# Performance work log

Hardware: AMD Instinct MI355X
Metric: run time of the kernel (lower is better)

## Reference

```python
import jax, jax.numpy as jnp
import numpy as np
import math

NB = 4           # num_bands
EPS = 1e-5       # LayerNorm eps


def _dwconv(x, w):
    # depthwise Conv1d, padding=1, kernel=3. x: [b, t, c], w: [c, 1, k]
    c = x.shape[-1]
    y = jax.lax.conv_general_dilated(
        x.transpose(0, 2, 1), w, window_strides=(1,), padding=[(1, 1)],
        dimension_numbers=('NCH', 'OIH', 'NCH'), feature_group_count=c)
    return y.transpose(0, 2, 1)


def _ln(x, g, b):
    m = jnp.mean(x, axis=-1, keepdims=True)
    v = jnp.mean(jnp.square(x - m), axis=-1, keepdims=True)
    return (x - m) * jax.lax.rsqrt(v + EPS) * g + b


def _attn(x, mem, qw, qc, kw, kc, vw, vc, ow, pw, prev_qk):
    # x, mem: [b, w, c]
    b, w, c = x.shape
    d = c // NB
    q = _dwconv(x @ qw.T, qc).reshape(b, w, NB, d).transpose(0, 2, 1, 3)      # [b,nb,w,d]
    k = _dwconv(mem @ kw.T, kc).reshape(b, w, NB, d).transpose(0, 2, 3, 1)    # [b,nb,d,w]
    v = _dwconv(mem @ vw.T, vc).reshape(b, w, NB, d).transpose(0, 2, 1, 3)    # [b,nb,w,d]
    # skewed relative-position bias: matmul + pad + transpose + slice
    p = jnp.einsum('bnwd,dt->bnwt', q, pw[:, :w])                              # [b,nb,w,w]
    p = jnp.pad(p, ((0, 0), (0, 0), (0, 0), (1, 0)))                           # pad last dim left
    p = p.transpose(0, 1, 3, 2)[:, :, 1:, :]                                   # skew
    qk = (jnp.einsum('bnwd,bndt->bnwt', q, k) + p) / math.sqrt(c)
    if prev_qk is not None:
        qk = qk + prev_qk
    a = jnp.einsum('bnwt,bntd->bnwd', jax.nn.softmax(qk, axis=-1), v)
    a = a.transpose(0, 2, 1, 3).reshape(b, w, c)
    return a @ ow.T, qk


def setup_inputs() -> dict:
    key = jax.random.key(0)
    ks = jax.random.split(key, 32)
    B, CH, BINS, W, FF = 4, 8, 1024, 1024, 2048
    s = 0.02
    inp = {
        'x': jax.random.normal(ks[0], (B, CH, BINS, W), jnp.float32),
        'mem': jax.random.normal(ks[1], (B, CH, BINS, W), jnp.float32),
        'prev_qk1': jax.random.normal(ks[2], (B, NB, W, W), jnp.float32),
        'prev_qk2': jax.random.normal(ks[3], (B, NB, W, W), jnp.float32),
        'ip_w': jax.random.normal(ks[4], (CH,), jnp.float32) * s,
        'ip_b': jnp.zeros((1,), jnp.float32),
        'mp_w': jax.random.normal(ks[5], (CH,), jnp.float32) * s,
        'mp_b': jnp.zeros((1,), jnp.float32),
        'ln1_g': jnp.ones((BINS,), jnp.float32), 'ln1_b': jnp.zeros((BINS,), jnp.float32),
        'ln2_g': jnp.ones((BINS,), jnp.float32), 'ln2_b': jnp.zeros((BINS,), jnp.float32),
        'ln3_g': jnp.ones((BINS,), jnp.float32), 'ln3_b': jnp.zeros((BINS,), jnp.float32),
        'a1_qw': jax.random.normal(ks[6], (BINS, BINS), jnp.float32) * s,
        'a1_qc': jax.random.normal(ks[7], (BINS, 1, 3), jnp.float32) * 0.3,
        'a1_kw': jax.random.normal(ks[8], (BINS, BINS), jnp.float32) * s,
        'a1_kc': jax.random.normal(ks[9], (BINS, 1, 3), jnp.float32) * 0.3,
        'a1_vw': jax.random.normal(ks[10], (BINS, BINS), jnp.float32) * s,
        'a1_vc': jax.random.normal(ks[11], (BINS, 1, 3), jnp.float32) * 0.3,
        'a1_ow': jax.random.normal(ks[12], (BINS, BINS), jnp.float32) * s,
        'a1_pw': jax.random.normal(ks[13], (BINS // NB, W), jnp.float32),
        'a2_qw': jax.random.normal(ks[14], (BINS, BINS), jnp.float32) * s,
        'a2_qc': jax.random.normal(ks[15], (BINS, 1, 3), jnp.float32) * 0.3,
        'a2_kw': jax.random.normal(ks[16], (BINS, BINS), jnp.float32) * s,
        'a2_kc': jax.random.normal(ks[17], (BINS, 1, 3), jnp.float32) * 0.3,
        'a2_vw': jax.random.normal(ks[18], (BINS, BINS), jnp.float32) * s,
        'a2_vc': jax.random.normal(ks[19], (BINS, 1, 3), jnp.float32) * 0.3,
        'a2_ow': jax.random.normal(ks[20], (BINS, BINS), jnp.float32) * s,
        'a2_pw': jax.random.normal(ks[21], (BINS // NB, W), jnp.float32),
        'l1_w': jax.random.normal(ks[22], (FF, BINS), jnp.float32) * s,
        'l2_w': jax.random.normal(ks[23], (BINS, FF), jnp.float32) * s,
    }
    return inp


def reference(x, mem, prev_qk1, prev_qk2, ip_w, ip_b, mp_w, mp_b,
              ln1_g, ln1_b, ln2_g, ln2_b, ln3_g, ln3_b,
              a1_qw, a1_qc, a1_kw, a1_kc, a1_vw, a1_vc, a1_ow, a1_pw,
              a2_qw, a2_qc, a2_kw, a2_kc, a2_vw, a2_vc, a2_ow, a2_pw,
              l1_w, l2_w):
    # 1x1 Conv2d to 1 channel then [b, w, bins] layout
    xs = jnp.einsum('bchw,c->bwh', x, ip_w) + ip_b    # [b, w, bins]
    ms = jnp.einsum('bchw,c->bwh', mem, mp_w) + mp_b
    # self-attention with prev_qk residual
    h, qk1 = _attn(_ln(xs, ln1_g, ln1_b), _ln(xs, ln1_g, ln1_b),
                   a1_qw, a1_qc, a1_kw, a1_kc, a1_vw, a1_vc, a1_ow, a1_pw, prev_qk1)
    xs = xs + h
    # cross-attention against mem
    h, qk2 = _attn(_ln(xs, ln2_g, ln2_b), ms,
                   a2_qw, a2_qc, a2_kw, a2_kc, a2_vw, a2_vc, a2_ow, a2_pw, prev_qk2)
    xs = xs + h
    # squared-ReLU FFN
    h = _ln(xs, ln3_g, ln3_b)
    h = jnp.square(jax.nn.relu(h @ l1_w.T)) @ l2_w.T
    xs = xs + h
    out = xs.transpose(0, 2, 1)[:, None]              # [b, 1, bins, w]
    return (out, qk1, qk2)
```

## Files before the change

### kernel.cpp

```cpp
#include <hip/hip_runtime.h>
#include <stdint.h>

typedef unsigned short u16;
typedef __bf16 bfv8 __attribute__((ext_vector_type(8)));
typedef float f32x4 __attribute__((ext_vector_type(4)));
typedef unsigned short u16x8 __attribute__((ext_vector_type(8)));

#define DI __device__ __forceinline__

DI u16 f2bf(float f) {
  union { float f; unsigned u; } c; c.f = f;
  unsigned r = c.u + 0x7FFFu + ((c.u >> 16) & 1u);
  return (u16)(r >> 16);
}
DI float bf2f(u16 b) {
  union { unsigned u; float f; } c; c.u = ((unsigned)b) << 16;
  return c.f;
}

enum { EPI_BF16 = 0, EPI_RELU2 = 1, EPI_ADDF32 = 2, EPI_QK = 3 };

#define GLDS(g, l)                                                              \
  __builtin_amdgcn_global_load_lds((const __attribute__((address_space(1))) void*)(g), \
                                   (__attribute__((address_space(3))) void*)(l), 16, 0, 0)

#define VMCNT_BAR(N)                                        \
  do {                                                      \
    asm volatile("s_waitcnt vmcnt(" #N ")" ::: "memory");   \
    __builtin_amdgcn_sched_barrier(0);                      \
    __builtin_amdgcn_s_barrier();                           \
    __builtin_amdgcn_sched_barrier(0);                      \
  } while (0)

template <int EPI, bool KSPLIT, int BN>
__global__ __launch_bounds__(512) void gemm256(
    const u16* __restrict__ Aq, const u16* __restrict__ Akv, int asplit,
    long a1q, long a1r, int lda1,
    const u16* __restrict__ A2, int lda2,
    const u16* __restrict__ B1, long b1q, long b1r, int ldb1,
    const u16* __restrict__ B2, long b2q, long b2r, int ldb2,
    int K, int ksp,
    void* __restrict__ Cv, long cq, long cr, int ldc,
    const float* __restrict__ extra, long eq, int lde,
    float scale)
{
  constexpr int NJ = BN / 64;
  constexpr int NBL = BN / 64;
  constexpr int SS = 8192 + BN * 64;
  constexpr int LPS = 2 + NBL;
  __shared__ __align__(16) u16 lds[3 * SS];
  const int tid = threadIdx.x;
  const int wid = tid >> 6, lane = tid & 63;

  const int gx = gridDim.x, gy = gridDim.y;
  const int nwg = gx * gy * (int)gridDim.z;
  const int flat = blockIdx.x + gx * (blockIdx.y + gy * blockIdx.z);
  const int q = nwg >> 3, r = nwg & 7;
  const int xcd = flat & 7, idx = flat >> 3;
  const int wg = (xcd < r ? xcd * (q + 1) : r * (q + 1) + (xcd - r) * q) + idx;
  const int bx = wg % gx;
  const int tmp = wg / gx;
  const int by = tmp % gy;
  const int bz = tmp / gy;

  const long zq = bz >> 2, zr = bz & 3;
  const int m0 = by * 128, n0 = bx * BN;
  const u16* Ab = ((n0 >= asplit) ? Akv : Aq) + zq * a1q + zr * a1r;
  const u16* Bb = B1 + zq * b1q + zr * b1r;
  const u16* B2b = KSPLIT ? (B2 + zq * b2q + zr * b2r) : (const u16*)nullptr;
  const int wm = (wid >> 2) * 64, wn = (wid & 3) * (BN / 4);
  const int fr = lane & 15, fq = lane >> 4;

  f32x4 acc[4][NJ];
#pragma unroll
  for (int i = 0; i < 4; ++i)
#pragma unroll
    for (int j = 0; j < NJ; ++j)
      acc[i][j] = (f32x4){0.f, 0.f, 0.f, 0.f};

  const int nt = K >> 6;

  auto STAGE = [&](int tt, int sb) {
    const int k0 = tt << 6;
    u16* Ld = &lds[sb * SS];
    const u16* Asrc; int la; const u16* Bsrc; int lb;
    if (!KSPLIT || k0 < ksp) { Asrc = Ab + k0; la = lda1; Bsrc = Bb + k0; lb = ldb1; }
    else { Asrc = A2 + (k0 - ksp); la = lda2; Bsrc = B2b + (k0 - ksp); lb = ldb2; }
#pragma unroll
    for (int l = 0; l < 2; ++l) {
      int idx2 = (l << 9) + tid;
      int row = idx2 >> 3;
      int sc = ((idx2 & 7) ^ (row & 7)) << 3;
      GLDS(Asrc + (size_t)(m0 + row) * la + sc,
           Ld + (((l << 3) + wid) << 9));
    }
#pragma unroll
    for (int l = 0; l < NBL; ++l) {
      int idx2 = (l << 9) + tid;
      int row = idx2 >> 3;
      int sc = ((idx2 & 7) ^ (row & 7)) << 3;
      GLDS(Bsrc + (size_t)(n0 + row) * lb + sc,
           Ld + 8192 + (((l << 3) + wid) << 9));
    }
  };

  auto COMPUTE = [&](int cb) {
    const u16* As = &lds[cb * SS];
    const u16* Bs = As + 8192;
#pragma unroll
    for (int ks = 0; ks < 2; ++ks) {
      bfv8 av[4];
#pragma unroll
      for (int i = 0; i < 4; ++i) {
        int ra = wm + i * 16 + fr;
        int ca = (((ks << 2) + fq) ^ (ra & 7)) << 3;
        av[i] = *(const bfv8*)&As[(ra << 6) + ca];
      }
#pragma unroll
      for (int nh = 0; nh < NJ / 2; ++nh) {
        bfv8 bv[2];
#pragma unroll
        for (int j = 0; j < 2; ++j) {
          int rb = wn + (nh << 5) + (j << 4) + fr;
          int cb2 = (((ks << 2) + fq) ^ (rb & 7)) << 3;
          bv[j] = *(const bfv8*)&Bs[(rb << 6) + cb2];
        }
        __builtin_amdgcn_s_setprio(1);
#pragma unroll
        for (int i = 0; i < 4; ++i) {
          acc[i][(nh << 1)] = __builtin_amdgcn_mfma_f32_16x16x32_bf16(av[i], bv[0], acc[i][(nh << 1)], 0, 0, 0);
          acc[i][(nh << 1) + 1] = __builtin_amdgcn_mfma_f32_16x16x32_bf16(av[i], bv[1], acc[i][(nh << 1) + 1], 0, 0, 0);
        }
        __builtin_amdgcn_s_setprio(0);
      }
    }
  };

  STAGE(0, 0);
  STAGE(1, 1);
  if constexpr (LPS == 6) VMCNT_BAR(6); else VMCNT_BAR(4);
  int cur = 0;
  for (int t = 0; t < nt; ++t) {
    if (t + 2 < nt) {
      int stg = cur + 2; if (stg >= 3) stg -= 3;
      STAGE(t + 2, stg);
      COMPUTE(cur);
      if constexpr (LPS == 6) VMCNT_BAR(6); else VMCNT_BAR(4);
    } else if (t + 1 < nt) {
      COMPUTE(cur);
      VMCNT_BAR(0);
    } else {
      COMPUTE(cur);
    }
    cur = (cur == 2) ? 0 : cur + 1;
  }

  if constexpr (EPI == EPI_BF16 || EPI == EPI_RELU2) {
    u16* Cb = (u16*)Cv + zq * cq + zr * cr;
#pragma unroll
    for (int i = 0; i < 4; ++i)
#pragma unroll
      for (int j = 0; j < NJ; ++j)
#pragma unroll
        for (int r2 = 0; r2 < 4; ++r2) {
          int row = m0 + wm + i * 16 + (fq << 2) + r2;
          int col = n0 + wn + j * 16 + fr;
          float v = acc[i][j][r2];
          if constexpr (EPI == EPI_RELU2) { v = fmaxf(v, 0.f); v = v * v; }
          Cb[(size_t)row * ldc + col] = f2bf(v);
        }
  } else if constexpr (EPI == EPI_ADDF32) {
    float* Cb = (float*)Cv + zq * cq + zr * cr;
#pragma unroll
    for (int i = 0; i < 4; ++i)
#pragma unroll
      for (int j = 0; j < NJ; ++j)
#pragma unroll
        for (int r2 = 0; r2 < 4; ++r2) {
          int row = m0 + wm + i * 16 + (fq << 2) + r2;
          int col = n0 + wn + j * 16 + fr;
          Cb[(size_t)row * ldc + col] += acc[i][j][r2];
        }
  } else {
    float* Cb = (float*)Cv + zq * cq + zr * cr;
    const float* Eb = extra + (size_t)bz * eq;
#pragma unroll
    for (int i = 0; i < 4; ++i)
#pragma unroll
      for (int j = 0; j < NJ; ++j)
#pragma unroll
        for (int r2 = 0; r2 < 4; ++r2) {
          int row = m0 + wm + i * 16 + (fq << 2) + r2;
          int col = n0 + wn + j * 16 + fr;
          Cb[(size_t)row * ldc + col] = acc[i][j][r2] * scale + Eb[(size_t)row * lde + col];
        }
  }
}

__global__ __launch_bounds__(1024) void proj3_kernel(const float* __restrict__ x,
                                                     const float* __restrict__ memp,
                                                     const float* __restrict__ ipw,
                                                     const float* __restrict__ ipb,
                                                     const float* __restrict__ mpw,
                                                     const float* __restrict__ mpb,
                                                     float* __restrict__ xs,
                                                     u16* __restrict__ msb)
{
  __shared__ f32x4 lt[16][256];
  const int task = blockIdx.z;
  const int b = blockIdx.y;
  const int h0 = blockIdx.x * 16;
  const float* src = task ? memp : x;
  const float* w8 = task ? mpw : ipw;
  const float bias = task ? mpb[0] : ipb[0];
  const int t = threadIdx.x;
  const int w4 = t & 255, hl = t >> 8;
  float wr[8];
#pragma unroll
  for (int c = 0; c < 8; ++c) wr[c] = w8[c];
#pragma unroll
  for (int p = 0; p < 4; ++p) {
    const int hr = p * 4 + hl;
    const size_t rowbase = ((size_t)b * 8 * 1024 + (h0 + hr)) * 1024 + (w4 << 2);
    f32x4 acc = {bias, bias, bias, bias};
#pragma unroll
    for (int c = 0; c < 8; ++c) {
      f32x4 v = *(const f32x4*)&src[rowbase + (size_t)c * 1048576];
      acc.x += v.x * wr[c]; acc.y += v.y * wr[c]; acc.z += v.z * wr[c]; acc.w += v.w * wr[c];
    }
    lt[hr][w4] = acc;
  }
  __syncthreads();
  const int w = t;
  float o[16];
#pragma unroll
  for (int h = 0; h < 16; ++h)
    o[h] = ((const float*)&lt[h][0])[w];
  if (task) {
    u16* d = &msb[((size_t)b * 1024 + w) * 1024 + h0];
    u16x8 o0, o1;
#pragma unroll
    for (int h = 0; h < 8; ++h) { o0[h] = f2bf(o[h]); o1[h] = f2bf(o[h + 8]); }
    *(u16x8*)&d[0] = o0;
    *(u16x8*)&d[8] = o1;
  } else {
    float* d = &xs[((size_t)b * 1024 + w) * 1024 + h0];
#pragma unroll
    for (int p = 0; p < 4; ++p) {
      f32x4 v = {o[p * 4], o[p * 4 + 1], o[p * 4 + 2], o[p * 4 + 3]};
      *(f32x4*)&d[p * 4] = v;
    }
  }
}

__global__ __launch_bounds__(256) void ln_kernel(const float* __restrict__ x,
                                                 const float* __restrict__ g,
                                                 const float* __restrict__ b,
                                                 u16* __restrict__ out)
{
  int row = blockIdx.x, tid = threadIdx.x;
  float4 v = ((const float4*)(x + (size_t)row * 1024))[tid];
  float s = v.x + v.y + v.z + v.w;
  float s2 = v.x * v.x + v.y * v.y + v.z * v.z + v.w * v.w;
#pragma unroll
  for (int o = 32; o; o >>= 1) { s += __shfl_down(s, o); s2 += __shfl_down(s2, o); }
  __shared__ float rs[4], rs2[4];
  int wid = tid >> 6, lane = tid & 63;
  if (lane == 0) { rs[wid] = s; rs2[wid] = s2; }
  __syncthreads();
  s = rs[0] + rs[1] + rs[2] + rs[3];
  s2 = rs2[0] + rs2[1] + rs2[2] + rs2[3];
  float mean = s * (1.f / 1024.f);
  float var = s2 * (1.f / 1024.f) - mean * mean;
  float rstd = rsqrtf(var + 1e-5f);
  float4 gv = ((const float4*)g)[tid];
  float4 bv = ((const float4*)b)[tid];
  ushort4 o;
  o.x = f2bf((v.x - mean) * rstd * gv.x + bv.x);
  o.y = f2bf((v.y - mean) * rstd * gv.y + bv.y);
  o.z = f2bf((v.z - mean) * rstd * gv.z + bv.z);
  o.w = f2bf((v.w - mean) * rstd * gv.w + bv.w);
  ((ushort4*)out)[(size_t)row * 256 + tid] = o;
}

__global__ __launch_bounds__(128) void dwconv_qk_kernel(const u16* __restrict__ qkv,
                                                        const float* __restrict__ qc,
                                                        const float* __restrict__ kc,
                                                        u16* __restrict__ Qc,
                                                        u16* __restrict__ Kc)
{
  int sel = blockIdx.y;
  int row = blockIdx.x;
  int t = row & 1023;
  int c0 = threadIdx.x * 8;
  const u16* r0 = qkv + (size_t)row * 3072 + (sel << 10) + c0;
  const float* wc = sel ? kc : qc;
  u16* dst = (sel ? Kc : Qc) + (size_t)row * 1024 + c0;
  u16x8 zv = {0, 0, 0, 0, 0, 0, 0, 0};
  u16x8 xm = zv, xp = zv;
  if (t > 0) xm = *(const u16x8*)(r0 - 3072);
  u16x8 xc = *(const u16x8*)r0;
  if (t < 1023) xp = *(const u16x8*)(r0 + 3072);
  u16x8 o;
#pragma unroll
  for (int j = 0; j < 8; ++j) {
    int c = c0 + j;
    float v = bf2f(xm[j]) * wc[c * 3 + 0] + bf2f(xc[j]) * wc[c * 3 + 1] + bf2f(xp[j]) * wc[c * 3 + 2];
    o[j] = f2bf(v);
  }
  *(u16x8*)dst = o;
}

__global__ __launch_bounds__(1024) void dwconv_t_kernel(const u16* __restrict__ qkv,
                                                        const float* __restrict__ wc,
                                                        u16* __restrict__ out)
{
  __shared__ float tile[32][33];
  int b = blockIdx.z;
  int t = blockIdx.x * 32 + threadIdx.y;
  int c = blockIdx.y * 32 + threadIdx.x;
  size_t base = ((size_t)b * 1024 + t) * 3072 + 2048 + c;
  float xm = (t > 0) ? bf2f(qkv[base - 3072]) : 0.f;
  float xc = bf2f(qkv[base]);
  float xp = (t < 1023) ? bf2f(qkv[base + 3072]) : 0.f;
  tile[threadIdx.y][threadIdx.x] = xm * wc[c * 3 + 0] + xc * wc[c * 3 + 1] + xp * wc[c * 3 + 2];
  __syncthreads();
  int c2 = blockIdx.y * 32 + threadIdx.y;
  int t2 = blockIdx.x * 32 + threadIdx.x;
  int z = b * 4 + (c2 >> 8);
  out[((size_t)z * 256 + (c2 & 255)) * 1024 + t2] = f2bf(tile[threadIdx.x][threadIdx.y]);
}

__global__ __launch_bounds__(256) void softmax_kernel(const float* __restrict__ qk,
                                                      u16* __restrict__ P)
{
  size_t row = blockIdx.x;
  int tid = threadIdx.x;
  float4 v = ((const float4*)(qk + row * 1024))[tid];
  float m = fmaxf(fmaxf(v.x, v.y), fmaxf(v.z, v.w));
#pragma unroll
  for (int o = 32; o; o >>= 1) m = fmaxf(m, __shfl_down(m, o));
  __shared__ float red[4];
  int wid = tid >> 6, lane = tid & 63;
  if (lane == 0) red[wid] = m;
  __syncthreads();
  m = fmaxf(fmaxf(red[0], red[1]), fmaxf(red[2], red[3]));
  float e0 = __expf(v.x - m), e1 = __expf(v.y - m), e2 = __expf(v.z - m), e3 = __expf(v.w - m);
  float s = e0 + e1 + e2 + e3;
#pragma unroll
  for (int o = 32; o; o >>= 1) s += __shfl_down(s, o);
  __syncthreads();
  if (lane == 0) red[wid] = s;
  __syncthreads();
  s = red[0] + red[1] + red[2] + red[3];
  float rinv = 1.f / s;
  ushort4 o;
  o.x = f2bf(e0 * rinv); o.y = f2bf(e1 * rinv); o.z = f2bf(e2 * rinv); o.w = f2bf(e3 * rinv);
  ((ushort4*)P)[row * 256 + tid] = o;
}

struct CastJobs { const float* s[12]; u16* d[12]; };
__global__ __launch_bounds__(256) void cast12_kernel(CastJobs J)
{
  int j = blockIdx.y;
  int i = blockIdx.x * 256 + threadIdx.x;
  float4 v = ((const float4*)J.s[j])[i];
  ushort4 o;
  o.x = f2bf(v.x); o.y = f2bf(v.y); o.z = f2bf(v.z); o.w = f2bf(v.w);
  ((ushort4*)J.d[j])[i] = o;
}

__global__ __launch_bounds__(1024) void pwt_kernel(const float* __restrict__ pw,
                                                   u16* __restrict__ pwT)
{
  __shared__ float tile[32][33];
  int d = blockIdx.y * 32 + threadIdx.y;
  int t = blockIdx.x * 32 + threadIdx.x;
  tile[threadIdx.y][threadIdx.x] = pw[(size_t)d * 1024 + t];
  __syncthreads();
  int t2 = blockIdx.x * 32 + threadIdx.y;
  int d2 = blockIdx.y * 32 + threadIdx.x;
  pwT[(size_t)t2 * 256 + d2] = f2bf(tile[threadIdx.x][threadIdx.y]);
}

__global__ __launch_bounds__(1024) void tout_kernel(const float* __restrict__ xs,
                                                    float* __restrict__ out)
{
  __shared__ float tile[32][33];
  int b = blockIdx.z;
  int w = blockIdx.x * 32 + threadIdx.y;
  int h = blockIdx.y * 32 + threadIdx.x;
  tile[threadIdx.y][threadIdx.x] = xs[((size_t)b * 1024 + w) * 1024 + h];
  __syncthreads();
  int h2 = blockIdx.y * 32 + threadIdx.y;
  int w2 = blockIdx.x * 32 + threadIdx.x;
  out[((size_t)b * 1024 + h2) * 1024 + w2] = tile[threadIdx.x][threadIdx.y];
}

static void run_attn(hipStream_t stream, float* xs, const u16* qsrc, const u16* kvsrc, int asplit,
                     u16* QKVraw, u16* Qc, u16* Kc, u16* Vt, u16* P, u16* Am,
                     const u16* wqkv, const u16* wo, const u16* pwt,
                     const float* qc, const float* kc, const float* vc,
                     const float* prevqk, float* qko)
{
  dim3 blk(512);
  gemm256<EPI_BF16, false, 256><<<dim3(12, 32, 1), blk, 0, stream>>>(
      qsrc, kvsrc, asplit, 0, 0, 1024, nullptr, 0,
      wqkv, 0, 0, 1024, nullptr, 0, 0, 0,
      1024, 0, QKVraw, 0, 0, 3072, nullptr, 0, 0, 1.f);
  dwconv_qk_kernel<<<dim3(4096, 2), 128, 0, stream>>>(QKVraw, qc, kc, Qc, Kc);
  dwconv_t_kernel<<<dim3(32, 32, 4), dim3(32, 32), 0, stream>>>(QKVraw, vc, Vt);
  gemm256<EPI_QK, true, 256><<<dim3(4, 8, 16), blk, 0, stream>>>(
      Qc, Qc, 1 << 30, 1048576, 256, 1024, pwt, 256,
      Kc, 1048576, 256, 1024, Qc, 1048576, 256, 1024,
      512, 256, qko, 4194304, 1048576, 1024, prevqk, 1048576, 1024, 0.03125f);
  softmax_kernel<<<16384, 256, 0, stream>>>(qko, P);
  gemm256<EPI_BF16, false, 128><<<dim3(2, 8, 16), blk, 0, stream>>>(
      P, P, 1 << 30, 4194304, 1048576, 1024, nullptr, 0,
      Vt, 1048576, 262144, 1024, nullptr, 0, 0, 0,
      1024, 0, Am, 1048576, 256, 1024, nullptr, 0, 0, 1.f);
  gemm256<EPI_ADDF32, false, 128><<<dim3(8, 32, 1), blk, 0, stream>>>(
      Am, Am, 1 << 30, 0, 0, 1024, nullptr, 0,
      wo, 0, 0, 1024, nullptr, 0, 0, 0,
      1024, 0, xs, 0, 0, 1024, nullptr, 0, 0, 1.f);
}

extern "C" void kernel_launch(void* const* d_in, const int* in_sizes, int n_in,
                              void* d_out, int out_size, void* d_ws, size_t ws_size,
                              hipStream_t stream)
{
  (void)in_sizes; (void)n_in; (void)out_size; (void)ws_size;
  const float* x    = (const float*)d_in[0];
  const float* memp = (const float*)d_in[1];
  const float* pqk1 = (const float*)d_in[2];
  const float* pqk2 = (const float*)d_in[3];
  const float* ip_w = (const float*)d_in[4];
  const float* ip_b = (const float*)d_in[5];
  const float* mp_w = (const float*)d_in[6];
  const float* mp_b = (const float*)d_in[7];
  const float* ln1g = (const float*)d_in[8];
  const float* ln1b = (const float*)d_in[9];
  const float* ln2g = (const float*)d_in[10];
  const float* ln2b = (const float*)d_in[11];
  const float* ln3g = (const float*)d_in[12];
  const float* ln3b = (const float*)d_in[13];
  const float* a1qw = (const float*)d_in[14];
  const float* a1qc = (const float*)d_in[15];
  const float* a1kw = (const float*)d_in[16];
  const float* a1kc = (const float*)d_in[17];
  const float* a1vw = (const float*)d_in[18];
  const float* a1vc = (const float*)d_in[19];
  const float* a1ow = (const float*)d_in[20];
  const float* a1pw = (const float*)d_in[21];
  const float* a2qw = (const float*)d_in[22];
  const float* a2qc = (const float*)d_in[23];
  const float* a2kw = (const float*)d_in[24];
  const float* a2kc = (const float*)d_in[25];
  const float* a2vw = (const float*)d_in[26];
  const float* a2vc = (const float*)d_in[27];
  const float* a2ow = (const float*)d_in[28];
  const float* a2pw = (const float*)d_in[29];
  const float* l1w  = (const float*)d_in[30];
  const float* l2w  = (const float*)d_in[31];

  float* outp = (float*)d_out;
  float* qk1o = outp + 4194304;
  float* qk2o = outp + 20971520;

  const size_t MB = 1024 * 1024;
  char* W = (char*)d_ws;
  float* xs   = (float*)(W);
  u16* msb    = (u16*)(W + 16 * MB);
  u16* xln    = (u16*)(W + 24 * MB);
  u16* QKVraw = (u16*)(W + 32 * MB);
  u16* Qc     = (u16*)(W + 56 * MB);
  u16* Kc     = (u16*)(W + 64 * MB);
  u16* Vt     = (u16*)(W + 72 * MB);
  u16* P      = (u16*)(W + 80 * MB);
  u16* Am     = (u16*)(W + 112 * MB);
  u16* wqkv1  = (u16*)(W + 120 * MB);
  u16* wqkv2  = (u16*)(W + 126 * MB);
  u16* wo1    = (u16*)(W + 132 * MB);
  u16* wo2    = (u16*)(W + 134 * MB);
  u16* wl1    = (u16*)(W + 136 * MB);
  u16* wl2    = (u16*)(W + 140 * MB);
  u16* pwt1   = (u16*)(W + 144 * MB);
  u16* pwt2   = (u16*)(W + 144 * MB + 512 * 1024);
  u16* H1     = QKVraw;

  CastJobs J;
  J.s[0] = a1qw; J.d[0] = wqkv1;
  J.s[1] = a1kw; J.d[1] = wqkv1 + 1048576;
  J.s[2] = a1vw; J.d[2] = wqkv1 + 2097152;
  J.s[3] = a2qw; J.d[3] = wqkv2;
  J.s[4] = a2kw; J.d[4] = wqkv2 + 1048576;
  J.s[5] = a2vw; J.d[5] = wqkv2 + 2097152;
  J.s[6] = a1ow; J.d[6] = wo1;
  J.s[7] = a2ow; J.d[7] = wo2;
  J.s[8] = l1w;            J.d[8] = wl1;
  J.s[9] = l1w + 1048576;  J.d[9] = wl1 + 1048576;
  J.s[10] = l2w;           J.d[10] = wl2;
  J.s[11] = l2w + 1048576; J.d[11] = wl2 + 1048576;
  cast12_kernel<<<dim3(1024, 12), 256, 0, stream>>>(J);
  pwt_kernel<<<dim3(32, 8, 1), dim3(32, 32), 0, stream>>>(a1pw, pwt1);
  pwt_kernel<<<dim3(32, 8, 1), dim3(32, 32), 0, stream>>>(a2pw, pwt2);

  proj3_kernel<<<dim3(64, 4, 2), 1024, 0, stream>>>(
      x, memp, ip_w, ip_b, mp_w, mp_b, xs, msb);

  ln_kernel<<<4096, 256, 0, stream>>>(xs, ln1g, ln1b, xln);
  run_attn(stream, xs, xln, xln, 1 << 30, QKVraw, Qc, Kc, Vt, P, Am,
           wqkv1, wo1, pwt1, a1qc, a1kc, a1vc, pqk1, qk1o);

  ln_kernel<<<4096, 256, 0, stream>>>(xs, ln2g, ln2b, xln);
  run_attn(stream, xs, xln, msb, 1024, QKVraw, Qc, Kc, Vt, P, Am,
           wqkv2, wo2, pwt2, a2qc, a2kc, a2vc, pqk2, qk2o);

  ln_kernel<<<4096, 256, 0, stream>>>(xs, ln3g, ln3b, xln);
  gemm256<EPI_RELU2, false, 256><<<dim3(8, 32, 1), dim3(512), 0, stream>>>(
      xln, xln, 1 << 30, 0, 0, 1024, nullptr, 0,
      wl1, 0, 0, 1024, nullptr, 0, 0, 0,
      1024, 0, H1, 0, 0, 2048, nullptr, 0, 0, 1.f);
  gemm256<EPI_ADDF32, false, 128><<<dim3(8, 32, 1), dim3(512), 0, stream>>>(
      H1, H1, 1 << 30, 0, 0, 2048, nullptr, 0,
      wl2, 0, 0, 2048, nullptr, 0, 0, 0,
      2048, 0, xs, 0, 0, 1024, nullptr, 0, 0, 1.f);

  tout_kernel<<<dim3(32, 32, 4), dim3(32, 32), 0, stream>>>(xs, outp);
}
```

Measured before the change: 515.3 us.

## Restructure input projection into double-buffered LDS-staged channel loop

Replaces the projection kernel with a smaller-block version that streams each input channel into LDS through direct global-to-LDS loads, double-buffered across the 8 channels. The kernel accumulates 16 rows per thread in registers and rotates the channel start order per block to spread DRAM traffic. The grid has more, smaller blocks, which should raise occupancy and overlap loads with compute. In exchange it adds extra barriers per channel and makes the code more complex.

```diff
diff --git a/kernel.cpp b/kernel.cpp
--- a/kernel.cpp
+++ b/kernel.cpp
@@ -27,6 +27,13 @@
 #define VMCNT_BAR(N)                                        \
   do {                                                      \
     asm volatile("s_waitcnt vmcnt(" #N ")" ::: "memory");   \
+    __builtin_amdgcn_sched_barrier(0);                      \
+    __builtin_amdgcn_s_barrier();                           \
+    __builtin_amdgcn_sched_barrier(0);                      \
+  } while (0)
+
+#define BAR_ONLY()                                          \
+  do {                                                      \
     __builtin_amdgcn_sched_barrier(0);                      \
     __builtin_amdgcn_s_barrier();                           \
     __builtin_amdgcn_sched_barrier(0);                      \
@@ -197,57 +204,72 @@
   }
 }
 
-__global__ __launch_bounds__(1024) void proj3_kernel(const float* __restrict__ x,
-                                                     const float* __restrict__ memp,
-                                                     const float* __restrict__ ipw,
-                                                     const float* __restrict__ ipb,
-                                                     const float* __restrict__ mpw,
-                                                     const float* __restrict__ mpb,
-                                                     float* __restrict__ xs,
-                                                     u16* __restrict__ msb)
-{
-  __shared__ f32x4 lt[16][256];
-  const int task = blockIdx.z;
-  const int b = blockIdx.y;
-  const int h0 = blockIdx.x * 16;
+__global__ __launch_bounds__(256) void proj4_kernel(const float* __restrict__ x,
+                                                    const float* __restrict__ memp,
+                                                    const float* __restrict__ ipw,
+                                                    const float* __restrict__ ipb,
+                                                    const float* __restrict__ mpw,
+                                                    const float* __restrict__ mpb,
+                                                    float* __restrict__ xs,
+                                                    u16* __restrict__ msb)
+{
+  __shared__ __align__(16) float sbuf[2][16][256];
+  const int t = threadIdx.x;
+  const int wid = t >> 6, lane = t & 63;
+  const int task = blockIdx.z >> 2;
+  const int b = blockIdx.z & 3;
+  const int h0 = blockIdx.x << 4;
+  const int w0 = blockIdx.y << 8;
   const float* src = task ? memp : x;
   const float* w8 = task ? mpw : ipw;
   const float bias = task ? mpb[0] : ipb[0];
-  const int t = threadIdx.x;
-  const int w4 = t & 255, hl = t >> 8;
+  const int crot = (blockIdx.x + blockIdx.y + blockIdx.z) & 7;
   float wr[8];
 #pragma unroll
-  for (int c = 0; c < 8; ++c) wr[c] = w8[c];
-#pragma unroll
-  for (int p = 0; p < 4; ++p) {
-    const int hr = p * 4 + hl;
-    const size_t rowbase = ((size_t)b * 8 * 1024 + (h0 + hr)) * 1024 + (w4 << 2);
-    f32x4 acc = {bias, bias, bias, bias};
-#pragma unroll
-    for (int c = 0; c < 8; ++c) {
-      f32x4 v = *(const f32x4*)&src[rowbase + (size_t)c * 1048576];
-      acc.x += v.x * wr[c]; acc.y += v.y * wr[c]; acc.z += v.z * wr[c]; acc.w += v.w * wr[c];
-    }
-    lt[hr][w4] = acc;
+  for (int j = 0; j < 8; ++j) wr[j] = w8[(j + crot) & 7];
+  float acc[16];
+#pragma unroll
+  for (int h = 0; h < 16; ++h) acc[h] = bias;
+  const size_t bbase = ((size_t)b * 8) << 20;
+
+  auto STAGE_C = [&](int i, int sb) {
+    const int c = (i + crot) & 7;
+    const float* g = src + bbase + ((size_t)c << 20) + (size_t)h0 * 1024 + w0 + (lane << 2);
+#pragma unroll
+    for (int l = 0; l < 4; ++l) {
+      int row = (wid << 2) + l;
+      GLDS(g + (size_t)row * 1024, &sbuf[sb][row][0]);
+    }
+  };
+
+  STAGE_C(0, 0);
+  STAGE_C(1, 1);
+#pragma unroll
+  for (int i = 0; i < 8; ++i) {
+    if (i < 7) VMCNT_BAR(4); else VMCNT_BAR(0);
+    {
+      const float wc = wr[i];
+      const int sb = i & 1;
+#pragma unroll
+      for (int h = 0; h < 16; ++h)
+        acc[h] += sbuf[sb][h][t] * wc;
+    }
+    BAR_ONLY();
+    if (i + 2 < 8) STAGE_C(i + 2, i & 1);
   }
-  __syncthreads();
-  const int w = t;
-  float o[16];
-#pragma unroll
-  for (int h = 0; h < 16; ++h)
-    o[h] = ((const float*)&lt[h][0])[w];
+
   if (task) {
-    u16* d = &msb[((size_t)b * 1024 + w) * 1024 + h0];
+    u16* d = &msb[((size_t)b * 1024 + w0 + t) * 1024 + h0];
     u16x8 o0, o1;
 #pragma unroll
-    for (int h = 0; h < 8; ++h) { o0[h] = f2bf(o[h]); o1[h] = f2bf(o[h + 8]); }
+    for (int h = 0; h < 8; ++h) { o0[h] = f2bf(acc[h]); o1[h] = f2bf(acc[h + 8]); }
     *(u16x8*)&d[0] = o0;
     *(u16x8*)&d[8] = o1;
   } else {
-    float* d = &xs[((size_t)b * 1024 + w) * 1024 + h0];
+    float* d = &xs[((size_t)b * 1024 + w0 + t) * 1024 + h0];
 #pragma unroll
     for (int p = 0; p < 4; ++p) {
-      f32x4 v = {o[p * 4], o[p * 4 + 1], o[p * 4 + 2], o[p * 4 + 3]};
+      f32x4 v = {acc[p * 4], acc[p * 4 + 1], acc[p * 4 + 2], acc[p * 4 + 3]};
       *(f32x4*)&d[p * 4] = v;
     }
   }
@@ -505,7 +527,7 @@
   pwt_kernel<<<dim3(32, 8, 1), dim3(32, 32), 0, stream>>>(a1pw, pwt1);
   pwt_kernel<<<dim3(32, 8, 1), dim3(32, 32), 0, stream>>>(a2pw, pwt2);
 
-  proj3_kernel<<<dim3(64, 4, 2), 1024, 0, stream>>>(
+  proj4_kernel<<<dim3(64, 4, 8), 256, 0, stream>>>(
       x, memp, ip_w, ip_b, mp_w, mp_b, xs, msb);
 
   ln_kernel<<<4096, 256, 0, stream>>>(xs, ln1g, ln1b, xln);
```

New measurement: 503.1 us. 1.02x faster.
